# Kernel tuning notes

Hardware: AMD Instinct MI355X
Metric: run time of the kernel (lower is better)

The kernel has to match this reference:

```python
import jax, jax.numpy as jnp
import numpy as np

_ALPHA_EPS = 1e-6


def _ema_weight_matrices(raw_alpha, T, dtype):
    """Return (K, T, T) row-normalized causal EMA weight matrices.

    W[k, t, s] = alpha_k^(t-s) / Z_t for s <= t, else 0, with Z_t the row sum.
    Computed in log space exactly like the torch reference.
    """
    alpha = jax.nn.sigmoid(raw_alpha).astype(dtype)
    alpha_safe = jnp.clip(alpha, _ALPHA_EPS, 1.0 - _ALPHA_EPS)  # (K,)
    idx = jnp.arange(T, dtype=dtype)
    diffs = idx[:, None] - idx[None, :]          # (T, T), t - s
    causal = diffs >= 0
    log_alpha = jnp.log(alpha_safe)              # (K,)
    log_W = log_alpha[:, None, None] * jnp.maximum(diffs, 0.0)  # (K, T, T)
    neg_inf = jnp.array(-jnp.inf, dtype=dtype)
    log_W = jnp.where(causal[None, :, :], log_W, neg_inf)
    log_Z = jax.nn.logsumexp(log_W, axis=2, keepdims=True)      # (K, T, 1)
    return jnp.exp(log_W - log_Z)                # (K, T, T)


def setup_inputs() -> dict:
    key = jax.random.key(0)
    k1, k2 = jax.random.split(key)
    B, T, d, K = 4, 4096, 512, 4
    h = jax.random.normal(k1, (B, T, d), dtype=jnp.float32)
    raw_alpha = jax.random.normal(k2, (K,), dtype=jnp.float32)
    return {"h": h, "raw_alpha": raw_alpha}


def reference(h, raw_alpha):
    """h: (B, T, d), raw_alpha: (K,) -> xis: (B, T, K, d)."""
    T = h.shape[1]
    W = _ema_weight_matrices(raw_alpha, T, h.dtype)   # (K, T, T)
    # per-channel causal weighted EMA: xi[b,t,k,:] = sum_s W[k,t,s] * h[b,s,:]
    return jnp.einsum('kts,bsd->btkd', W, h)
```

## Files before the change

kernel.cpp:

```cpp
#include <hip/hip_runtime.h>
#include <math.h>


namespace {

constexpr int T_LEN  = 4096;
constexpr int D_DIM  = 512;
constexpr int D4     = D_DIM / 4;
constexpr int K_CH   = 4;
constexpr int CHUNK  = 32;
constexpr int NCHUNK = T_LEN / CHUNK;

__device__ __forceinline__ float sigmoid_clip(float x) {
    float a = 1.0f / (1.0f + expf(-x));
    return fminf(fmaxf(a, 1e-6f), 1.0f - 1e-6f);
}

__global__ void ema_chunk_sums(const float4* __restrict__ h4,
                               const float*  __restrict__ raw_alpha,
                               float4* __restrict__ lbuf) {
    const int c  = blockIdx.x % NCHUNK;
    const int b  = blockIdx.x / NCHUNK;
    const int d4 = threadIdx.x;

    float al[K_CH];
#pragma unroll
    for (int k = 0; k < K_CH; ++k) al[k] = sigmoid_clip(raw_alpha[k]);

    float4 acc[K_CH];
#pragma unroll
    for (int k = 0; k < K_CH; ++k) acc[k] = make_float4(0.f, 0.f, 0.f, 0.f);

    const float4* hp = h4 + ((size_t)b * T_LEN + (size_t)c * CHUNK) * D4 + d4;
    for (int j = 0; j < CHUNK; ++j) {
        float4 hv = hp[(size_t)j * D4];
#pragma unroll
        for (int k = 0; k < K_CH; ++k) {
            acc[k].x = fmaf(al[k], acc[k].x, hv.x);
            acc[k].y = fmaf(al[k], acc[k].y, hv.y);
            acc[k].z = fmaf(al[k], acc[k].z, hv.z);
            acc[k].w = fmaf(al[k], acc[k].w, hv.w);
        }
    }
#pragma unroll
    for (int k = 0; k < K_CH; ++k) {
        lbuf[(((size_t)b * NCHUNK + c) * K_CH + k) * D4 + d4] = acc[k];
    }
}

__global__ void ema_chunk_scan(const float* __restrict__ raw_alpha,
                               float4* __restrict__ buf, int total) {
    const int idx = blockIdx.x * blockDim.x + threadIdx.x;
    if (idx >= total) return;
    const int d4 = idx % D4;
    const int k  = (idx / D4) % K_CH;
    const int b  = idx / (D4 * K_CH);

    const float a  = sigmoid_clip(raw_alpha[k]);
    const float aC = exp2f((float)CHUNK * log2f(a));

    float4 pre = make_float4(0.f, 0.f, 0.f, 0.f);
    for (int c = 0; c < NCHUNK; ++c) {
        const size_t off = (((size_t)b * NCHUNK + c) * K_CH + k) * D4 + d4;
        const float4 L = buf[off];
        buf[off] = pre;
        pre.x = fmaf(aC, pre.x, L.x);
        pre.y = fmaf(aC, pre.y, L.y);
        pre.z = fmaf(aC, pre.z, L.z);
        pre.w = fmaf(aC, pre.w, L.w);
    }
}

__global__ void ema_apply(const float4* __restrict__ h4,
                          const float*  __restrict__ raw_alpha,
                          const float4* __restrict__ pbuf,
                          float4* __restrict__ out4) {
    const int c  = blockIdx.x % NCHUNK;
    const int b  = blockIdx.x / NCHUNK;
    const int d4 = threadIdx.x;
    const int t0 = c * CHUNK;

    float al[K_CH], om[K_CH], pw[K_CH];
#pragma unroll
    for (int k = 0; k < K_CH; ++k) {
        const float a = sigmoid_clip(raw_alpha[k]);
        al[k] = a;
        om[k] = 1.0f - a;
        pw[k] = exp2f((float)(t0 + 1) * log2f(a));
    }

    float4 S[K_CH];
#pragma unroll
    for (int k = 0; k < K_CH; ++k)
        S[k] = pbuf[(((size_t)b * NCHUNK + c) * K_CH + k) * D4 + d4];

    const float4* hp = h4 + ((size_t)b * T_LEN + t0) * D4 + d4;
    float4* op = out4 + (((size_t)b * T_LEN + t0) * (size_t)K_CH) * D4 + d4;

    for (int j = 0; j < CHUNK; ++j) {
        const float4 hv = hp[(size_t)j * D4];
#pragma unroll
        for (int k = 0; k < K_CH; ++k) {
            S[k].x = fmaf(al[k], S[k].x, hv.x);
            S[k].y = fmaf(al[k], S[k].y, hv.y);
            S[k].z = fmaf(al[k], S[k].z, hv.z);
            S[k].w = fmaf(al[k], S[k].w, hv.w);
            const float invZ = om[k] / fmaxf(1.0f - pw[k], 1e-30f);
            float4 o;
            o.x = S[k].x * invZ;
            o.y = S[k].y * invZ;
            o.z = S[k].z * invZ;
            o.w = S[k].w * invZ;
            op[((size_t)j * K_CH + k) * D4] = o;
            pw[k] *= al[k];
        }
    }
}

}

extern "C" void kernel_launch(void* const* d_in, const int* in_sizes, int n_in,
                              void* d_out, int out_size, void* d_ws, size_t ws_size,
                              hipStream_t stream) {
    const float* h         = (const float*)d_in[0];
    const float* raw_alpha = (const float*)d_in[1];
    float* out = (float*)d_out;

    const int B = in_sizes[0] / (T_LEN * D_DIM);

    float4* lbuf = (float4*)d_ws;

    const dim3 blk(D4);
    const dim3 grid1(B * NCHUNK);

    hipLaunchKernelGGL(ema_chunk_sums, grid1, blk, 0, stream,
                       (const float4*)h, raw_alpha, lbuf);

    const int total = B * K_CH * D4;
    hipLaunchKernelGGL(ema_chunk_scan, dim3((total + 255) / 256), dim3(256), 0, stream,
                       raw_alpha, lbuf, total);

    hipLaunchKernelGGL(ema_apply, grid1, blk, 0, stream,
                       (const float4*)h, raw_alpha, (const float4*)lbuf, (float4*)out);
}
```

Measured before the change: 50.88 us.

## Fuse chunk-sum, scan and apply into one cooperative kernel with register-held inputs

Replaces the three kernel launches with one cooperative kernel that uses grid-wide syncs between phases. Each block keeps its 32-row chunk of h in registers, so h is read once instead of twice. The serial per-channel chunk scan becomes a two-level hierarchical scan over groups of 8 chunks, which removes the long sequential 128-step loop. In exchange it needs 512 co-resident blocks, two grid barriers, heavy register pressure from holding 32 float4 values per thread, and redundant prefix reads in every block.

```diff
diff --git a/kernel.cpp b/kernel.cpp
--- a/kernel.cpp
+++ b/kernel.cpp
@@ -1,5 +1,8 @@
 #include <hip/hip_runtime.h>
+#include <hip/hip_cooperative_groups.h>
 #include <math.h>
+
+namespace cg = cooperative_groups;
 
 
 namespace {
@@ -10,101 +13,122 @@
 constexpr int K_CH   = 4;
 constexpr int CHUNK  = 32;
 constexpr int NCHUNK = T_LEN / CHUNK;
+constexpr int GRP    = 8;
+constexpr int NGRP   = NCHUNK / GRP;
 
 __device__ __forceinline__ float sigmoid_clip(float x) {
     float a = 1.0f / (1.0f + expf(-x));
     return fminf(fmaxf(a, 1e-6f), 1.0f - 1e-6f);
 }
 
-__global__ void ema_chunk_sums(const float4* __restrict__ h4,
-                               const float*  __restrict__ raw_alpha,
-                               float4* __restrict__ lbuf) {
-    const int c  = blockIdx.x % NCHUNK;
-    const int b  = blockIdx.x / NCHUNK;
-    const int d4 = threadIdx.x;
-
-    float al[K_CH];
-#pragma unroll
-    for (int k = 0; k < K_CH; ++k) al[k] = sigmoid_clip(raw_alpha[k]);
-
-    float4 acc[K_CH];
-#pragma unroll
-    for (int k = 0; k < K_CH; ++k) acc[k] = make_float4(0.f, 0.f, 0.f, 0.f);
-
-    const float4* hp = h4 + ((size_t)b * T_LEN + (size_t)c * CHUNK) * D4 + d4;
-    for (int j = 0; j < CHUNK; ++j) {
-        float4 hv = hp[(size_t)j * D4];
-#pragma unroll
-        for (int k = 0; k < K_CH; ++k) {
-            acc[k].x = fmaf(al[k], acc[k].x, hv.x);
-            acc[k].y = fmaf(al[k], acc[k].y, hv.y);
-            acc[k].z = fmaf(al[k], acc[k].z, hv.z);
-            acc[k].w = fmaf(al[k], acc[k].w, hv.w);
-        }
-    }
-#pragma unroll
-    for (int k = 0; k < K_CH; ++k) {
-        lbuf[(((size_t)b * NCHUNK + c) * K_CH + k) * D4 + d4] = acc[k];
-    }
+__device__ __forceinline__ void fma4(float4& d, float a, const float4& x) {
+    d.x = fmaf(a, d.x, x.x);
+    d.y = fmaf(a, d.y, x.y);
+    d.z = fmaf(a, d.z, x.z);
+    d.w = fmaf(a, d.w, x.w);
 }
 
-__global__ void ema_chunk_scan(const float* __restrict__ raw_alpha,
-                               float4* __restrict__ buf, int total) {
-    const int idx = blockIdx.x * blockDim.x + threadIdx.x;
-    if (idx >= total) return;
-    const int d4 = idx % D4;
-    const int k  = (idx / D4) % K_CH;
-    const int b  = idx / (D4 * K_CH);
-
-    const float a  = sigmoid_clip(raw_alpha[k]);
-    const float aC = exp2f((float)CHUNK * log2f(a));
-
-    float4 pre = make_float4(0.f, 0.f, 0.f, 0.f);
-    for (int c = 0; c < NCHUNK; ++c) {
-        const size_t off = (((size_t)b * NCHUNK + c) * K_CH + k) * D4 + d4;
-        const float4 L = buf[off];
-        buf[off] = pre;
-        pre.x = fmaf(aC, pre.x, L.x);
-        pre.y = fmaf(aC, pre.y, L.y);
-        pre.z = fmaf(aC, pre.z, L.z);
-        pre.w = fmaf(aC, pre.w, L.w);
-    }
-}
-
-__global__ void ema_apply(const float4* __restrict__ h4,
-                          const float*  __restrict__ raw_alpha,
-                          const float4* __restrict__ pbuf,
-                          float4* __restrict__ out4) {
+__global__ void __launch_bounds__(128, 2)
+ema_fused(const float4* __restrict__ h4,
+          const float*  __restrict__ raw_alpha,
+          float4* __restrict__ lbuf,
+          float4* __restrict__ gbuf,
+          float4* __restrict__ out4,
+          int B)
+{
+    cg::grid_group grid = cg::this_grid();
     const int c  = blockIdx.x % NCHUNK;
     const int b  = blockIdx.x / NCHUNK;
     const int d4 = threadIdx.x;
     const int t0 = c * CHUNK;
 
-    float al[K_CH], om[K_CH], pw[K_CH];
+    float al[K_CH], aC[K_CH];
 #pragma unroll
     for (int k = 0; k < K_CH; ++k) {
-        const float a = sigmoid_clip(raw_alpha[k]);
-        al[k] = a;
-        om[k] = 1.0f - a;
-        pw[k] = exp2f((float)(t0 + 1) * log2f(a));
+        al[k] = sigmoid_clip(raw_alpha[k]);
+        aC[k] = exp2f((float)CHUNK * log2f(al[k]));
     }
+
+    float4 hreg[CHUNK];
+    {
+        const float4* hp = h4 + ((size_t)b * T_LEN + t0) * D4 + d4;
+#pragma unroll
+        for (int j = 0; j < CHUNK; ++j) hreg[j] = hp[(size_t)j * D4];
+    }
+    {
+        float4 L[K_CH];
+#pragma unroll
+        for (int k = 0; k < K_CH; ++k) L[k] = make_float4(0.f, 0.f, 0.f, 0.f);
+#pragma unroll
+        for (int j = 0; j < CHUNK; ++j) {
+#pragma unroll
+            for (int k = 0; k < K_CH; ++k) fma4(L[k], al[k], hreg[j]);
+        }
+#pragma unroll
+        for (int k = 0; k < K_CH; ++k)
+            lbuf[(((size_t)b * NCHUNK + c) * K_CH + k) * D4 + d4] = L[k];
+    }
+
+    grid.sync();
+
+    if (blockIdx.x < (unsigned)(B * NGRP)) {
+        const int g  = blockIdx.x % NGRP;
+        const int bb = blockIdx.x / NGRP;
+        float4 G[K_CH];
+#pragma unroll
+        for (int k = 0; k < K_CH; ++k) G[k] = make_float4(0.f, 0.f, 0.f, 0.f);
+        for (int i = 0; i < GRP; ++i) {
+            const int cp = g * GRP + i;
+#pragma unroll
+            for (int k = 0; k < K_CH; ++k) {
+                float4 Lv = lbuf[(((size_t)bb * NCHUNK + cp) * K_CH + k) * D4 + d4];
+                fma4(G[k], aC[k], Lv);
+            }
+        }
+#pragma unroll
+        for (int k = 0; k < K_CH; ++k)
+            gbuf[(((size_t)bb * NGRP + g) * K_CH + k) * D4 + d4] = G[k];
+    }
+
+    grid.sync();
 
     float4 S[K_CH];
 #pragma unroll
-    for (int k = 0; k < K_CH; ++k)
-        S[k] = pbuf[(((size_t)b * NCHUNK + c) * K_CH + k) * D4 + d4];
+    for (int k = 0; k < K_CH; ++k) S[k] = make_float4(0.f, 0.f, 0.f, 0.f);
+    {
+        const int g = c / GRP;
+        float aG[K_CH];
+#pragma unroll
+        for (int k = 0; k < K_CH; ++k)
+            aG[k] = exp2f((float)(CHUNK * GRP) * log2f(al[k]));
+        for (int gp = 0; gp < g; ++gp) {
+#pragma unroll
+            for (int k = 0; k < K_CH; ++k) {
+                float4 Gv = gbuf[(((size_t)b * NGRP + gp) * K_CH + k) * D4 + d4];
+                fma4(S[k], aG[k], Gv);
+            }
+        }
+        for (int cp = g * GRP; cp < c; ++cp) {
+#pragma unroll
+            for (int k = 0; k < K_CH; ++k) {
+                float4 Lv = lbuf[(((size_t)b * NCHUNK + cp) * K_CH + k) * D4 + d4];
+                fma4(S[k], aC[k], Lv);
+            }
+        }
+    }
 
-    const float4* hp = h4 + ((size_t)b * T_LEN + t0) * D4 + d4;
+    float om[K_CH], pw[K_CH];
+#pragma unroll
+    for (int k = 0; k < K_CH; ++k) {
+        om[k] = 1.0f - al[k];
+        pw[k] = exp2f((float)(t0 + 1) * log2f(al[k]));
+    }
     float4* op = out4 + (((size_t)b * T_LEN + t0) * (size_t)K_CH) * D4 + d4;
-
+#pragma unroll
     for (int j = 0; j < CHUNK; ++j) {
-        const float4 hv = hp[(size_t)j * D4];
 #pragma unroll
         for (int k = 0; k < K_CH; ++k) {
-            S[k].x = fmaf(al[k], S[k].x, hv.x);
-            S[k].y = fmaf(al[k], S[k].y, hv.y);
-            S[k].z = fmaf(al[k], S[k].z, hv.z);
-            S[k].w = fmaf(al[k], S[k].w, hv.w);
+            fma4(S[k], al[k], hreg[j]);
             const float invZ = om[k] / fmaxf(1.0f - pw[k], 1e-30f);
             float4 o;
             o.x = S[k].x * invZ;
@@ -121,25 +145,19 @@
 
 extern "C" void kernel_launch(void* const* d_in, const int* in_sizes, int n_in,
                               void* d_out, int out_size, void* d_ws, size_t ws_size,
-                              hipStream_t stream) {
-    const float* h         = (const float*)d_in[0];
-    const float* raw_alpha = (const float*)d_in[1];
-    float* out = (float*)d_out;
+                              hipStream_t stream)
+{
+    const float4* h4        = (const float4*)d_in[0];
+    const float*  raw_alpha = (const float*)d_in[1];
+    float4* out4 = (float4*)d_out;
 
-    const int B = in_sizes[0] / (T_LEN * D_DIM);
+    int B = in_sizes[0] / (T_LEN * D_DIM);
 
     float4* lbuf = (float4*)d_ws;
+    float4* gbuf = lbuf + (size_t)B * NCHUNK * K_CH * D4;
 
-    const dim3 blk(D4);
-    const dim3 grid1(B * NCHUNK);
-
-    hipLaunchKernelGGL(ema_chunk_sums, grid1, blk, 0, stream,
-                       (const float4*)h, raw_alpha, lbuf);
-
-    const int total = B * K_CH * D4;
-    hipLaunchKernelGGL(ema_chunk_scan, dim3((total + 255) / 256), dim3(256), 0, stream,
-                       raw_alpha, lbuf, total);
-
-    hipLaunchKernelGGL(ema_apply, grid1, blk, 0, stream,
-                       (const float4*)h, raw_alpha, (const float4*)lbuf, (float4*)out);
+    void* kargs[] = { (void*)&h4, (void*)&raw_alpha, (void*)&lbuf,
+                      (void*)&gbuf, (void*)&out4, (void*)&B };
+    hipLaunchCooperativeKernel((void*)ema_fused, dim3(B * NCHUNK), dim3(D4),
+                               kargs, 0, stream);
 }
```

Result: slower. 151.4 us (+197.6%).

## Drop serial chunk-scan kernel; each apply block reduces preceding chunk sums itself

Applied to the files above, without the earlier changes.

Removes the middle kernel, which scanned 128 chunks serially with only 2048 threads. Each apply block now computes its own prefix state by folding all earlier chunk sums, weighted by alpha^CHUNK. That costs O(NCHUNK^2) redundant reads of the small chunk-sum buffer but saves one launch and the poorly parallel serial pass. Blocks are issued in reverse chunk order so the longest prefix loops start first, and launch bounds and unroll pragmas are added.

```diff
diff --git a/kernel.cpp b/kernel.cpp
--- a/kernel.cpp
+++ b/kernel.cpp
@@ -16,9 +16,17 @@
     return fminf(fmaxf(a, 1e-6f), 1.0f - 1e-6f);
 }
 
-__global__ void ema_chunk_sums(const float4* __restrict__ h4,
-                               const float*  __restrict__ raw_alpha,
-                               float4* __restrict__ lbuf) {
+__device__ __forceinline__ void fma4(float4& d, float a, const float4& x) {
+    d.x = fmaf(a, d.x, x.x);
+    d.y = fmaf(a, d.y, x.y);
+    d.z = fmaf(a, d.z, x.z);
+    d.w = fmaf(a, d.w, x.w);
+}
+
+__global__ void __launch_bounds__(128)
+ema_chunk_sums(const float4* __restrict__ h4,
+               const float*  __restrict__ raw_alpha,
+               float4* __restrict__ lbuf) {
     const int c  = blockIdx.x % NCHUNK;
     const int b  = blockIdx.x / NCHUNK;
     const int d4 = threadIdx.x;
@@ -32,79 +40,64 @@
     for (int k = 0; k < K_CH; ++k) acc[k] = make_float4(0.f, 0.f, 0.f, 0.f);
 
     const float4* hp = h4 + ((size_t)b * T_LEN + (size_t)c * CHUNK) * D4 + d4;
+#pragma unroll 4
     for (int j = 0; j < CHUNK; ++j) {
         float4 hv = hp[(size_t)j * D4];
 #pragma unroll
-        for (int k = 0; k < K_CH; ++k) {
-            acc[k].x = fmaf(al[k], acc[k].x, hv.x);
-            acc[k].y = fmaf(al[k], acc[k].y, hv.y);
-            acc[k].z = fmaf(al[k], acc[k].z, hv.z);
-            acc[k].w = fmaf(al[k], acc[k].w, hv.w);
-        }
+        for (int k = 0; k < K_CH; ++k) fma4(acc[k], al[k], hv);
     }
 #pragma unroll
-    for (int k = 0; k < K_CH; ++k) {
+    for (int k = 0; k < K_CH; ++k)
         lbuf[(((size_t)b * NCHUNK + c) * K_CH + k) * D4 + d4] = acc[k];
-    }
 }
 
-__global__ void ema_chunk_scan(const float* __restrict__ raw_alpha,
-                               float4* __restrict__ buf, int total) {
-    const int idx = blockIdx.x * blockDim.x + threadIdx.x;
-    if (idx >= total) return;
-    const int d4 = idx % D4;
-    const int k  = (idx / D4) % K_CH;
-    const int b  = idx / (D4 * K_CH);
-
-    const float a  = sigmoid_clip(raw_alpha[k]);
-    const float aC = exp2f((float)CHUNK * log2f(a));
-
-    float4 pre = make_float4(0.f, 0.f, 0.f, 0.f);
-    for (int c = 0; c < NCHUNK; ++c) {
-        const size_t off = (((size_t)b * NCHUNK + c) * K_CH + k) * D4 + d4;
-        const float4 L = buf[off];
-        buf[off] = pre;
-        pre.x = fmaf(aC, pre.x, L.x);
-        pre.y = fmaf(aC, pre.y, L.y);
-        pre.z = fmaf(aC, pre.z, L.z);
-        pre.w = fmaf(aC, pre.w, L.w);
-    }
-}
-
-__global__ void ema_apply(const float4* __restrict__ h4,
-                          const float*  __restrict__ raw_alpha,
-                          const float4* __restrict__ pbuf,
-                          float4* __restrict__ out4) {
-    const int c  = blockIdx.x % NCHUNK;
+__global__ void __launch_bounds__(128)
+ema_apply(const float4* __restrict__ h4,
+          const float*  __restrict__ raw_alpha,
+          const float4* __restrict__ lbuf,
+          float4* __restrict__ out4) {
+    const int c  = (NCHUNK - 1) - (blockIdx.x % NCHUNK);
     const int b  = blockIdx.x / NCHUNK;
     const int d4 = threadIdx.x;
     const int t0 = c * CHUNK;
 
-    float al[K_CH], om[K_CH], pw[K_CH];
+    float al[K_CH], aC[K_CH];
 #pragma unroll
     for (int k = 0; k < K_CH; ++k) {
-        const float a = sigmoid_clip(raw_alpha[k]);
-        al[k] = a;
-        om[k] = 1.0f - a;
-        pw[k] = exp2f((float)(t0 + 1) * log2f(a));
+        al[k] = sigmoid_clip(raw_alpha[k]);
+        aC[k] = exp2f((float)CHUNK * log2f(al[k]));
     }
 
     float4 S[K_CH];
 #pragma unroll
-    for (int k = 0; k < K_CH; ++k)
-        S[k] = pbuf[(((size_t)b * NCHUNK + c) * K_CH + k) * D4 + d4];
+    for (int k = 0; k < K_CH; ++k) S[k] = make_float4(0.f, 0.f, 0.f, 0.f);
+
+    const float4* lp = lbuf + ((size_t)b * NCHUNK * K_CH) * D4 + d4;
+#pragma unroll 4
+    for (int cp = 0; cp < c; ++cp) {
+#pragma unroll
+        for (int k = 0; k < K_CH; ++k) {
+            float4 Lv = lp[((size_t)cp * K_CH + k) * D4];
+            fma4(S[k], aC[k], Lv);
+        }
+    }
+
+    float om[K_CH], pw[K_CH];
+#pragma unroll
+    for (int k = 0; k < K_CH; ++k) {
+        om[k] = 1.0f - al[k];
+        pw[k] = exp2f((float)(t0 + 1) * log2f(al[k]));
+    }
 
     const float4* hp = h4 + ((size_t)b * T_LEN + t0) * D4 + d4;
     float4* op = out4 + (((size_t)b * T_LEN + t0) * (size_t)K_CH) * D4 + d4;
 
+#pragma unroll 2
     for (int j = 0; j < CHUNK; ++j) {
         const float4 hv = hp[(size_t)j * D4];
 #pragma unroll
         for (int k = 0; k < K_CH; ++k) {
-            S[k].x = fmaf(al[k], S[k].x, hv.x);
-            S[k].y = fmaf(al[k], S[k].y, hv.y);
-            S[k].z = fmaf(al[k], S[k].z, hv.z);
-            S[k].w = fmaf(al[k], S[k].w, hv.w);
+            fma4(S[k], al[k], hv);
             const float invZ = om[k] / fmaxf(1.0f - pw[k], 1e-30f);
             float4 o;
             o.x = S[k].x * invZ;
@@ -121,25 +114,21 @@
 
 extern "C" void kernel_launch(void* const* d_in, const int* in_sizes, int n_in,
                               void* d_out, int out_size, void* d_ws, size_t ws_size,
-                              hipStream_t stream) {
-    const float* h         = (const float*)d_in[0];
-    const float* raw_alpha = (const float*)d_in[1];
-    float* out = (float*)d_out;
+                              hipStream_t stream)
+{
+    const float4* h4        = (const float4*)d_in[0];
+    const float*  raw_alpha = (const float*)d_in[1];
+    float4* out4 = (float4*)d_out;
 
     const int B = in_sizes[0] / (T_LEN * D_DIM);
 
     float4* lbuf = (float4*)d_ws;
 
     const dim3 blk(D4);
-    const dim3 grid1(B * NCHUNK);
+    const dim3 grid(B * NCHUNK);
 
-    hipLaunchKernelGGL(ema_chunk_sums, grid1, blk, 0, stream,
-                       (const float4*)h, raw_alpha, lbuf);
-
-    const int total = B * K_CH * D4;
-    hipLaunchKernelGGL(ema_chunk_scan, dim3((total + 255) / 256), dim3(256), 0, stream,
-                       raw_alpha, lbuf, total);
-
-    hipLaunchKernelGGL(ema_apply, grid1, blk, 0, stream,
-                       (const float4*)h, raw_alpha, (const float4*)lbuf, (float4*)out);
+    hipLaunchKernelGGL(ema_chunk_sums, grid, blk, 0, stream,
+                       h4, raw_alpha, lbuf);
+    hipLaunchKernelGGL(ema_apply, grid, blk, 0, stream,
+                       h4, raw_alpha, lbuf, out4);
 }
```

Measured after the change: 78.75 us. 1.55x slower.
